# Kernel optimization log

Hardware: AMD Instinct MI355X
Metric: run time of the kernel (lower is better)

## Reference

```python
import jax, jax.numpy as jnp
import numpy as np

NUM_HEADS = 8

def _mha(x, Wq, Wk, Wv, Wo):
    # x: (..., S, C); standard multi-head self-attention, no bias, no dropout (eval mode)
    C = x.shape[-1]
    dh = C // NUM_HEADS
    lead = x.shape[:-1]
    q = (x @ Wq.T).reshape(*lead, NUM_HEADS, dh)
    k = (x @ Wk.T).reshape(*lead, NUM_HEADS, dh)
    v = (x @ Wv.T).reshape(*lead, NUM_HEADS, dh)
    scores = jnp.einsum('...qhd,...khd->...hqk', q, k) * (dh ** -0.5)
    attn = jax.nn.softmax(scores, axis=-1)
    o = jnp.einsum('...hqk,...khd->...qhd', attn, v).reshape(*lead, C)
    return o @ Wo.T

def _axial_block(xs, Wq_h, Wk_h, Wv_h, Wo_h, Wq_w, Wk_w, Wv_w, Wo_w):
    # xs: (B, C, H, W)
    # height attention: sequence along H, batched over (B, W)
    xh = jnp.transpose(xs, (0, 3, 2, 1))            # (B, W, H, C)
    oh = _mha(xh, Wq_h, Wk_h, Wv_h, Wo_h)           # (B, W, H, C)
    oh = jnp.transpose(oh, (0, 3, 2, 1))            # (B, C, H, W)
    # width attention: sequence along W, batched over (B, H)
    xw = jnp.transpose(xs, (0, 2, 3, 1))            # (B, H, W, C)
    ow = _mha(xw, Wq_w, Wk_w, Wv_w, Wo_w)           # (B, H, W, C)
    ow = jnp.transpose(ow, (0, 3, 1, 2))            # (B, C, H, W)
    return xs + oh + ow

def setup_inputs() -> dict:
    key = jax.random.key(0)
    ks = jax.random.split(key, 9)
    B, C, H, W = 8, 512, 128, 128
    s = C ** -0.5
    xs = jax.random.normal(ks[0], (B, C, H, W), dtype=jnp.float32)
    names = ['Wq_h', 'Wk_h', 'Wv_h', 'Wo_h', 'Wq_w', 'Wk_w', 'Wv_w', 'Wo_w']
    ws = {n: jax.random.normal(k, (C, C), dtype=jnp.float32) * s for n, k in zip(names, ks[1:])}
    return {'xs': xs, **ws}

def reference(xs, Wq_h, Wk_h, Wv_h, Wo_h, Wq_w, Wk_w, Wv_w, Wo_w):
    return _axial_block(xs, Wq_h, Wk_h, Wv_h, Wo_h, Wq_w, Wk_w, Wv_w, Wo_w)
```

## Files before the change

kernel.cpp:

```cpp
#include <hip/hip_runtime.h>

#define CC   512
#define HWT  16384
#define NB   8
#define DH   64
#define SEQ  128

typedef __bf16 bf16_t;
typedef __bf16 bf16x8 __attribute__((ext_vector_type(8)));
typedef float  f32x4  __attribute__((ext_vector_type(4)));

__global__ __launch_bounds__(256) void prep_w_kernel(const float* __restrict__ W0,
                                                     const float* __restrict__ W1,
                                                     const float* __restrict__ W2,
                                                     const float* __restrict__ W3,
                                                     const float* __restrict__ W4,
                                                     const float* __restrict__ W5,
                                                     const float* __restrict__ W6,
                                                     const float* __restrict__ W7,
                                                     bf16_t* __restrict__ Wb) {
  const float* Wsrc[8] = {W0, W1, W2, W3, W4, W5, W6, W7};
  const int w = blockIdx.y;
  const int i = (blockIdx.x * 256 + threadIdx.x) * 4;
  float4 v = *(const float4*)(Wsrc[w] + i);
  bf16_t* o = Wb + (size_t)w * (CC * CC) + i;
  o[0] = (bf16_t)v.x; o[1] = (bf16_t)v.y; o[2] = (bf16_t)v.z; o[3] = (bf16_t)v.w;
}

__global__ __launch_bounds__(256) void t0_kernel(const float* __restrict__ xs,
                                                 bf16_t* __restrict__ Xt) {
  __shared__ bf16_t T[64 * 72];
  const int hw0 = blockIdx.x * 64, c0 = blockIdx.y * 64;
  const size_t boff = (size_t)blockIdx.z * CC * HWT;
  const int t = threadIdx.x;
  for (int p = 0; p < 4; p++) {
    int job = t + p * 256;
    int c_l = job >> 4, ch = job & 15;
    float4 v = *(const float4*)(xs + boff + (size_t)(c0 + c_l) * HWT + hw0 + ch * 4);
    T[(ch * 4 + 0) * 72 + c_l] = (bf16_t)v.x;
    T[(ch * 4 + 1) * 72 + c_l] = (bf16_t)v.y;
    T[(ch * 4 + 2) * 72 + c_l] = (bf16_t)v.z;
    T[(ch * 4 + 3) * 72 + c_l] = (bf16_t)v.w;
  }
  __syncthreads();
  for (int p = 0; p < 2; p++) {
    int job = t + p * 256;
    int hw_l = job >> 3, ch = job & 7;
    uint4 v = *(const uint4*)&T[hw_l * 72 + ch * 8];
    *(uint4*)(Xt + boff + (size_t)(hw0 + hw_l) * CC + c0 + ch * 8) = v;
  }
}

__global__ __launch_bounds__(256) void gemm_kernel(const bf16_t* __restrict__ A,
                                                   const bf16_t* __restrict__ Wt,
                                                   bf16_t* __restrict__ D) {
  __shared__ bf16_t As[128 * 40];
  __shared__ bf16_t Ws[128 * 40];
  const int m0 = blockIdx.x * 128, n0 = blockIdx.y * 128;
  const size_t boff = (size_t)blockIdx.z * HWT * CC;
  const bf16_t* Ab = A + boff;
  bf16_t* Db = D + boff;
  const int t = threadIdx.x;
  const int lane = t & 63, wv = t >> 6;
  const int wy = wv >> 1, wx = wv & 1;
  const int r_l = t >> 2, kcol = (t & 3) * 8;
  const int ln15 = lane & 15, q8 = (lane >> 4) * 8;

  f32x4 acc[4][4];
  for (int i = 0; i < 4; i++)
    for (int j = 0; j < 4; j++) acc[i][j] = {0.f, 0.f, 0.f, 0.f};

  for (int kb = 0; kb < 16; kb++) {
    const int kk = kb * 32 + kcol;
    uint4 a0 = *(const uint4*)(Ab + (size_t)(m0 + r_l) * CC + kk);
    uint4 a1 = *(const uint4*)(Ab + (size_t)(m0 + r_l + 64) * CC + kk);
    uint4 w0 = *(const uint4*)(Wt + (size_t)(n0 + r_l) * CC + kk);
    uint4 w1 = *(const uint4*)(Wt + (size_t)(n0 + r_l + 64) * CC + kk);
    __syncthreads();
    *(uint4*)&As[r_l * 40 + kcol] = a0;
    *(uint4*)&As[(r_l + 64) * 40 + kcol] = a1;
    *(uint4*)&Ws[r_l * 40 + kcol] = w0;
    *(uint4*)&Ws[(r_l + 64) * 40 + kcol] = w1;
    __syncthreads();
    bf16x8 af[4], wf[4];
    for (int i = 0; i < 4; i++)
      af[i] = *(const bf16x8*)&As[(wy * 64 + i * 16 + ln15) * 40 + q8];
    for (int j = 0; j < 4; j++)
      wf[j] = *(const bf16x8*)&Ws[(wx * 64 + j * 16 + ln15) * 40 + q8];
    for (int i = 0; i < 4; i++)
      for (int j = 0; j < 4; j++)
        acc[i][j] = __builtin_amdgcn_mfma_f32_16x16x32_bf16(af[i], wf[j], acc[i][j], 0, 0, 0);
  }

  const int qr = (lane >> 4) * 4;
  for (int i = 0; i < 4; i++)
    for (int j = 0; j < 4; j++) {
      const int row = m0 + wy * 64 + i * 16 + qr;
      const int col = n0 + wx * 64 + j * 16 + ln15;
      for (int r = 0; r < 4; r++)
        Db[(size_t)(row + r) * CC + col] = (bf16_t)acc[i][j][r];
    }
}

__global__ __launch_bounds__(256) void attn_kernel(const bf16_t* __restrict__ Q,
                                                   const bf16_t* __restrict__ K,
                                                   const bf16_t* __restrict__ V,
                                                   bf16_t* __restrict__ O,
                                                   int seq_stride, int o_stride) {
  __shared__ bf16_t smem[128 * 72 * 2 + 64 * 136];
  bf16_t* Qs = smem;
  bf16_t* Ks = smem + 128 * 72;
  bf16_t* Vs = smem + 2 * 128 * 72;
  bf16_t* Ps = smem;

  const int o = blockIdx.x, head = blockIdx.y;
  const size_t base = (size_t)blockIdx.z * HWT * CC + (size_t)o * o_stride + head * 64;
  const int t = threadIdx.x, lane = t & 63, wv = t >> 6;
  const int ln15 = lane & 15, q = lane >> 4;

  for (int p = 0; p < 4; p++) {
    int job = t + p * 256;
    int s = job >> 3, ch = job & 7;
    uint4 qv = *(const uint4*)(Q + base + (size_t)s * seq_stride + ch * 8);
    uint4 kv = *(const uint4*)(K + base + (size_t)s * seq_stride + ch * 8);
    *(uint4*)&Qs[s * 72 + ch * 8] = qv;
    *(uint4*)&Ks[s * 72 + ch * 8] = kv;
  }
  for (int p = 0; p < 4; p++) {
    int job = t + p * 256;
    int s = job >> 3, ch = job & 7;
    uint4 vv = *(const uint4*)(V + base + (size_t)s * seq_stride + ch * 8);
    const bf16_t* e = (const bf16_t*)&vv;
    for (int jj = 0; jj < 8; jj++) Vs[(ch * 8 + jj) * 136 + s] = e[jj];
  }
  __syncthreads();

  f32x4 sacc[2][8];
  for (int i = 0; i < 2; i++)
    for (int j = 0; j < 8; j++) sacc[i][j] = {0.f, 0.f, 0.f, 0.f};
  for (int ks = 0; ks < 2; ks++) {
    bf16x8 qf[2], kf[8];
    for (int i = 0; i < 2; i++)
      qf[i] = *(const bf16x8*)&Qs[(wv * 32 + i * 16 + ln15) * 72 + ks * 32 + q * 8];
    for (int j = 0; j < 8; j++)
      kf[j] = *(const bf16x8*)&Ks[(j * 16 + ln15) * 72 + ks * 32 + q * 8];
    for (int i = 0; i < 2; i++)
      for (int j = 0; j < 8; j++)
        sacc[i][j] = __builtin_amdgcn_mfma_f32_16x16x32_bf16(qf[i], kf[j], sacc[i][j], 0, 0, 0);
  }
  __syncthreads();

  const float scale = 0.125f;
  float linv[2][4];
  for (int i = 0; i < 2; i++)
    for (int r = 0; r < 4; r++) {
      float m = -1e30f;
      for (int j = 0; j < 8; j++) m = fmaxf(m, sacc[i][j][r]);
      for (int d = 1; d < 16; d <<= 1) m = fmaxf(m, __shfl_xor(m, d));
      m *= scale;
      float sum = 0.f;
      for (int j = 0; j < 8; j++) {
        float pv = __expf(sacc[i][j][r] * scale - m);
        sacc[i][j][r] = pv;
        sum += pv;
      }
      for (int d = 1; d < 16; d <<= 1) sum += __shfl_xor(sum, d);
      linv[i][r] = 1.f / sum;
    }
  for (int i = 0; i < 2; i++)
    for (int j = 0; j < 8; j++)
      for (int r = 0; r < 4; r++)
        Ps[(wv * 32 + i * 16 + q * 4 + r) * 136 + j * 16 + ln15] = (bf16_t)sacc[i][j][r];
  __syncthreads();

  f32x4 oacc[2][4];
  for (int i = 0; i < 2; i++)
    for (int j = 0; j < 4; j++) oacc[i][j] = {0.f, 0.f, 0.f, 0.f};
  for (int ks = 0; ks < 4; ks++) {
    bf16x8 pf[2], vf[4];
    for (int i = 0; i < 2; i++)
      pf[i] = *(const bf16x8*)&Ps[(wv * 32 + i * 16 + ln15) * 136 + ks * 32 + q * 8];
    for (int j = 0; j < 4; j++)
      vf[j] = *(const bf16x8*)&Vs[(j * 16 + ln15) * 136 + ks * 32 + q * 8];
    for (int i = 0; i < 2; i++)
      for (int j = 0; j < 4; j++)
        oacc[i][j] = __builtin_amdgcn_mfma_f32_16x16x32_bf16(pf[i], vf[j], oacc[i][j], 0, 0, 0);
  }
  for (int i = 0; i < 2; i++)
    for (int j = 0; j < 4; j++)
      for (int r = 0; r < 4; r++) {
        const int s = wv * 32 + i * 16 + q * 4 + r;
        const int d = j * 16 + ln15;
        O[base + (size_t)s * seq_stride + d] = (bf16_t)(oacc[i][j][r] * linv[i][r]);
      }
}

__global__ __launch_bounds__(256) void final_add_kernel(const float* __restrict__ xs,
                                                        const bf16_t* __restrict__ OH,
                                                        const bf16_t* __restrict__ OW,
                                                        float* __restrict__ out) {
  __shared__ float TF[64 * 65];
  const int hw0 = blockIdx.x * 64, c0 = blockIdx.y * 64;
  const size_t boff = (size_t)blockIdx.z * CC * HWT;
  const int t = threadIdx.x;
  for (int p = 0; p < 2; p++) {
    int job = t + p * 256;
    int hw_l = job >> 3, ch = job & 7;
    size_t off = boff + (size_t)(hw0 + hw_l) * CC + c0 + ch * 8;
    bf16x8 a = *(const bf16x8*)(OH + off);
    bf16x8 b = *(const bf16x8*)(OW + off);
    for (int jj = 0; jj < 8; jj++)
      TF[(ch * 8 + jj) * 65 + hw_l] = (float)a[jj] + (float)b[jj];
  }
  __syncthreads();
  for (int p = 0; p < 4; p++) {
    int job = t + p * 256;
    int c_l = job >> 4, ch = job & 15;
    size_t off = boff + (size_t)(c0 + c_l) * HWT + hw0 + ch * 4;
    float4 xv = *(const float4*)(xs + off);
    float4 ov;
    ov.x = xv.x + TF[c_l * 65 + ch * 4 + 0];
    ov.y = xv.y + TF[c_l * 65 + ch * 4 + 1];
    ov.z = xv.z + TF[c_l * 65 + ch * 4 + 2];
    ov.w = xv.w + TF[c_l * 65 + ch * 4 + 3];
    *(float4*)(out + off) = ov;
  }
}

extern "C" void kernel_launch(void* const* d_in, const int* in_sizes, int n_in,
                              void* d_out, int out_size, void* d_ws, size_t ws_size,
                              hipStream_t stream) {
  const float* xs = (const float*)d_in[0];
  float* out = (float*)d_out;

  bf16_t* Wb = (bf16_t*)d_ws;
  const size_t wbytes = (size_t)8 * CC * CC * sizeof(bf16_t);
  bf16_t* wsb = Wb + (size_t)8 * CC * CC;

  const size_t pb = (size_t)HWT * CC;
  size_t avail = (ws_size > wbytes) ? (ws_size - wbytes) : 0;
  int chunkB = (int)(avail / (6 * pb * sizeof(bf16_t)));
  if (chunkB > NB) chunkB = NB;
  if (chunkB < 1) chunkB = 1;
  const size_t R = (size_t)chunkB * pb;
  bf16_t* Xt = wsb;
  bf16_t* Qb = wsb + R;
  bf16_t* Kb = wsb + 2 * R;
  bf16_t* Vb = wsb + 3 * R;
  bf16_t* Ab = wsb + 4 * R;
  bf16_t* OH = wsb + 5 * R;

  prep_w_kernel<<<dim3(CC * CC / 1024, 8), 256, 0, stream>>>(
      (const float*)d_in[1], (const float*)d_in[2], (const float*)d_in[3],
      (const float*)d_in[4], (const float*)d_in[5], (const float*)d_in[6],
      (const float*)d_in[7], (const float*)d_in[8], Wb);
  const bf16_t* Wq_h = Wb + 0 * (size_t)CC * CC;
  const bf16_t* Wk_h = Wb + 1 * (size_t)CC * CC;
  const bf16_t* Wv_h = Wb + 2 * (size_t)CC * CC;
  const bf16_t* Wo_h = Wb + 3 * (size_t)CC * CC;
  const bf16_t* Wq_w = Wb + 4 * (size_t)CC * CC;
  const bf16_t* Wk_w = Wb + 5 * (size_t)CC * CC;
  const bf16_t* Wv_w = Wb + 6 * (size_t)CC * CC;
  const bf16_t* Wo_w = Wb + 7 * (size_t)CC * CC;

  for (int b0 = 0; b0 < NB; b0 += chunkB) {
    const int cb = (NB - b0 < chunkB) ? (NB - b0) : chunkB;
    const float* xsc = xs + (size_t)b0 * pb;
    float* outc = out + (size_t)b0 * pb;
    dim3 gT(HWT / 64, CC / 64, cb);
    dim3 gG(HWT / 128, CC / 128, cb);
    dim3 gA(128, 8, cb);
    dim3 blk(256);

    t0_kernel<<<gT, blk, 0, stream>>>(xsc, Xt);
    gemm_kernel<<<gG, blk, 0, stream>>>(Xt, Wq_h, Qb);
    gemm_kernel<<<gG, blk, 0, stream>>>(Xt, Wk_h, Kb);
    gemm_kernel<<<gG, blk, 0, stream>>>(Xt, Wv_h, Vb);
    attn_kernel<<<gA, blk, 0, stream>>>(Qb, Kb, Vb, Ab, 128 * CC, CC);
    gemm_kernel<<<gG, blk, 0, stream>>>(Ab, Wo_h, OH);
    gemm_kernel<<<gG, blk, 0, stream>>>(Xt, Wq_w, Qb);
    gemm_kernel<<<gG, blk, 0, stream>>>(Xt, Wk_w, Kb);
    gemm_kernel<<<gG, blk, 0, stream>>>(Xt, Wv_w, Vb);
    attn_kernel<<<gA, blk, 0, stream>>>(Qb, Kb, Vb, Ab, CC, 128 * CC);
    gemm_kernel<<<gG, blk, 0, stream>>>(Ab, Wo_w, Xt);
    final_add_kernel<<<gT, blk, 0, stream>>>(xsc, OH, Xt, outc);
  }
}
```

Before: 1.732 ms.

## Fuse QKV projections into one GEMM and stage tiles via global_load_lds

Merges the three separate Q, K and V projection GEMMs into one GEMM with N=1536, relying on the three bf16 weight matrices sitting next to each other in the workspace. Q, K and V are written interleaved with row stride 1536, and the attention kernel takes separate input and output strides. The GEMM now copies A and W tiles straight from global memory into LDS with global_load_lds, dropping the register round trip and the padded LDS layout. The unpadded 32-element rows risk LDS bank conflicts on the fragment reads, and a second barrier per k-step is added.

```diff
diff --git a/kernel.cpp b/kernel.cpp
--- a/kernel.cpp
+++ b/kernel.cpp
@@ -5,10 +5,16 @@
 #define NB   8
 #define DH   64
 #define SEQ  128
+#define C3   1536
 
 typedef __bf16 bf16_t;
 typedef __bf16 bf16x8 __attribute__((ext_vector_type(8)));
 typedef float  f32x4  __attribute__((ext_vector_type(4)));
+
+#define GLOAD_LDS16(g, l)                                                      \
+  __builtin_amdgcn_global_load_lds(                                            \
+      (const __attribute__((address_space(1))) void*)(g),                      \
+      (__attribute__((address_space(3))) void*)(l), 16, 0, 0)
 
 __global__ __launch_bounds__(256) void prep_w_kernel(const float* __restrict__ W0,
                                                      const float* __restrict__ W1,
@@ -53,43 +59,45 @@
 
 __global__ __launch_bounds__(256) void gemm_kernel(const bf16_t* __restrict__ A,
                                                    const bf16_t* __restrict__ Wt,
-                                                   bf16_t* __restrict__ D) {
-  __shared__ bf16_t As[128 * 40];
-  __shared__ bf16_t Ws[128 * 40];
+                                                   bf16_t* __restrict__ D,
+                                                   int ldD) {
+  __shared__ bf16_t As[128 * 32];
+  __shared__ bf16_t Ws[128 * 32];
   const int m0 = blockIdx.x * 128, n0 = blockIdx.y * 128;
-  const size_t boff = (size_t)blockIdx.z * HWT * CC;
-  const bf16_t* Ab = A + boff;
-  bf16_t* Db = D + boff;
+  const bf16_t* Ab = A + (size_t)blockIdx.z * HWT * CC;
+  bf16_t* Db = D + (size_t)blockIdx.z * HWT * (size_t)ldD;
   const int t = threadIdx.x;
   const int lane = t & 63, wv = t >> 6;
   const int wy = wv >> 1, wx = wv & 1;
-  const int r_l = t >> 2, kcol = (t & 3) * 8;
   const int ln15 = lane & 15, q8 = (lane >> 4) * 8;
+
+  const int seg0 = wv * 2;
+  const int srow = lane >> 2;
+  const int scol = (lane & 3) * 8;
 
   f32x4 acc[4][4];
   for (int i = 0; i < 4; i++)
     for (int j = 0; j < 4; j++) acc[i][j] = {0.f, 0.f, 0.f, 0.f};
 
   for (int kb = 0; kb < 16; kb++) {
-    const int kk = kb * 32 + kcol;
-    uint4 a0 = *(const uint4*)(Ab + (size_t)(m0 + r_l) * CC + kk);
-    uint4 a1 = *(const uint4*)(Ab + (size_t)(m0 + r_l + 64) * CC + kk);
-    uint4 w0 = *(const uint4*)(Wt + (size_t)(n0 + r_l) * CC + kk);
-    uint4 w1 = *(const uint4*)(Wt + (size_t)(n0 + r_l + 64) * CC + kk);
-    __syncthreads();
-    *(uint4*)&As[r_l * 40 + kcol] = a0;
-    *(uint4*)&As[(r_l + 64) * 40 + kcol] = a1;
-    *(uint4*)&Ws[r_l * 40 + kcol] = w0;
-    *(uint4*)&Ws[(r_l + 64) * 40 + kcol] = w1;
+    const int kk = kb * 32;
+#pragma unroll
+    for (int i = 0; i < 2; i++) {
+      const int seg = seg0 + i;
+      const int row = seg * 16 + srow;
+      GLOAD_LDS16(Ab + (size_t)(m0 + row) * CC + kk + scol, &As[seg * 512]);
+      GLOAD_LDS16(Wt + (size_t)(n0 + row) * CC + kk + scol, &Ws[seg * 512]);
+    }
     __syncthreads();
     bf16x8 af[4], wf[4];
     for (int i = 0; i < 4; i++)
-      af[i] = *(const bf16x8*)&As[(wy * 64 + i * 16 + ln15) * 40 + q8];
+      af[i] = *(const bf16x8*)&As[(wy * 64 + i * 16 + ln15) * 32 + q8];
     for (int j = 0; j < 4; j++)
-      wf[j] = *(const bf16x8*)&Ws[(wx * 64 + j * 16 + ln15) * 40 + q8];
+      wf[j] = *(const bf16x8*)&Ws[(wx * 64 + j * 16 + ln15) * 32 + q8];
     for (int i = 0; i < 4; i++)
       for (int j = 0; j < 4; j++)
         acc[i][j] = __builtin_amdgcn_mfma_f32_16x16x32_bf16(af[i], wf[j], acc[i][j], 0, 0, 0);
+    __syncthreads();
   }
 
   const int qr = (lane >> 4) * 4;
@@ -98,7 +106,7 @@
       const int row = m0 + wy * 64 + i * 16 + qr;
       const int col = n0 + wx * 64 + j * 16 + ln15;
       for (int r = 0; r < 4; r++)
-        Db[(size_t)(row + r) * CC + col] = (bf16_t)acc[i][j][r];
+        Db[(size_t)(row + r) * ldD + col] = (bf16_t)acc[i][j][r];
     }
 }
 
@@ -106,7 +114,8 @@
                                                    const bf16_t* __restrict__ K,
                                                    const bf16_t* __restrict__ V,
                                                    bf16_t* __restrict__ O,
-                                                   int seq_stride, int o_stride) {
+                                                   int in_ss, int in_os, int in_bs,
+                                                   int out_ss, int out_os, int out_bs) {
   __shared__ bf16_t smem[128 * 72 * 2 + 64 * 136];
   bf16_t* Qs = smem;
   bf16_t* Ks = smem + 128 * 72;
@@ -114,22 +123,23 @@
   bf16_t* Ps = smem;
 
   const int o = blockIdx.x, head = blockIdx.y;
-  const size_t base = (size_t)blockIdx.z * HWT * CC + (size_t)o * o_stride + head * 64;
+  const size_t ibase = (size_t)blockIdx.z * in_bs + (size_t)o * in_os + head * 64;
+  const size_t obase = (size_t)blockIdx.z * out_bs + (size_t)o * out_os + head * 64;
   const int t = threadIdx.x, lane = t & 63, wv = t >> 6;
   const int ln15 = lane & 15, q = lane >> 4;
 
   for (int p = 0; p < 4; p++) {
     int job = t + p * 256;
     int s = job >> 3, ch = job & 7;
-    uint4 qv = *(const uint4*)(Q + base + (size_t)s * seq_stride + ch * 8);
-    uint4 kv = *(const uint4*)(K + base + (size_t)s * seq_stride + ch * 8);
+    uint4 qv = *(const uint4*)(Q + ibase + (size_t)s * in_ss + ch * 8);
+    uint4 kv = *(const uint4*)(K + ibase + (size_t)s * in_ss + ch * 8);
     *(uint4*)&Qs[s * 72 + ch * 8] = qv;
     *(uint4*)&Ks[s * 72 + ch * 8] = kv;
   }
   for (int p = 0; p < 4; p++) {
     int job = t + p * 256;
     int s = job >> 3, ch = job & 7;
-    uint4 vv = *(const uint4*)(V + base + (size_t)s * seq_stride + ch * 8);
+    uint4 vv = *(const uint4*)(V + ibase + (size_t)s * in_ss + ch * 8);
     const bf16_t* e = (const bf16_t*)&vv;
     for (int jj = 0; jj < 8; jj++) Vs[(ch * 8 + jj) * 136 + s] = e[jj];
   }
@@ -191,7 +201,7 @@
       for (int r = 0; r < 4; r++) {
         const int s = wv * 32 + i * 16 + q * 4 + r;
         const int d = j * 16 + ln15;
-        O[base + (size_t)s * seq_stride + d] = (bf16_t)(oacc[i][j][r] * linv[i][r]);
+        O[obase + (size_t)s * out_ss + d] = (bf16_t)(oacc[i][j][r] * linv[i][r]);
       }
 }
 
@@ -243,46 +253,41 @@
   if (chunkB > NB) chunkB = NB;
   if (chunkB < 1) chunkB = 1;
   const size_t R = (size_t)chunkB * pb;
-  bf16_t* Xt = wsb;
-  bf16_t* Qb = wsb + R;
-  bf16_t* Kb = wsb + 2 * R;
-  bf16_t* Vb = wsb + 3 * R;
-  bf16_t* Ab = wsb + 4 * R;
-  bf16_t* OH = wsb + 5 * R;
+  bf16_t* Xt  = wsb;
+  bf16_t* QKV = wsb + R;
+  bf16_t* Ab  = wsb + 4 * R;
+  bf16_t* OH  = wsb + 5 * R;
 
   prep_w_kernel<<<dim3(CC * CC / 1024, 8), 256, 0, stream>>>(
       (const float*)d_in[1], (const float*)d_in[2], (const float*)d_in[3],
       (const float*)d_in[4], (const float*)d_in[5], (const float*)d_in[6],
       (const float*)d_in[7], (const float*)d_in[8], Wb);
-  const bf16_t* Wq_h = Wb + 0 * (size_t)CC * CC;
-  const bf16_t* Wk_h = Wb + 1 * (size_t)CC * CC;
-  const bf16_t* Wv_h = Wb + 2 * (size_t)CC * CC;
-  const bf16_t* Wo_h = Wb + 3 * (size_t)CC * CC;
-  const bf16_t* Wq_w = Wb + 4 * (size_t)CC * CC;
-  const bf16_t* Wk_w = Wb + 5 * (size_t)CC * CC;
-  const bf16_t* Wv_w = Wb + 6 * (size_t)CC * CC;
-  const bf16_t* Wo_w = Wb + 7 * (size_t)CC * CC;
+  const bf16_t* Wqkv_h = Wb + 0 * (size_t)CC * CC;
+  const bf16_t* Wo_h   = Wb + 3 * (size_t)CC * CC;
+  const bf16_t* Wqkv_w = Wb + 4 * (size_t)CC * CC;
+  const bf16_t* Wo_w   = Wb + 7 * (size_t)CC * CC;
 
   for (int b0 = 0; b0 < NB; b0 += chunkB) {
     const int cb = (NB - b0 < chunkB) ? (NB - b0) : chunkB;
     const float* xsc = xs + (size_t)b0 * pb;
     float* outc = out + (size_t)b0 * pb;
     dim3 gT(HWT / 64, CC / 64, cb);
-    dim3 gG(HWT / 128, CC / 128, cb);
+    dim3 gQKV(HWT / 128, C3 / 128, cb);
+    dim3 gO(HWT / 128, CC / 128, cb);
     dim3 gA(128, 8, cb);
     dim3 blk(256);
 
     t0_kernel<<<gT, blk, 0, stream>>>(xsc, Xt);
-    gemm_kernel<<<gG, blk, 0, stream>>>(Xt, Wq_h, Qb);
-    gemm_kernel<<<gG, blk, 0, stream>>>(Xt, Wk_h, Kb);
-    gemm_kernel<<<gG, blk, 0, stream>>>(Xt, Wv_h, Vb);
-    attn_kernel<<<gA, blk, 0, stream>>>(Qb, Kb, Vb, Ab, 128 * CC, CC);
-    gemm_kernel<<<gG, blk, 0, stream>>>(Ab, Wo_h, OH);
-    gemm_kernel<<<gG, blk, 0, stream>>>(Xt, Wq_w, Qb);
-    gemm_kernel<<<gG, blk, 0, stream>>>(Xt, Wk_w, Kb);
-    gemm_kernel<<<gG, blk, 0, stream>>>(Xt, Wv_w, Vb);
-    attn_kernel<<<gA, blk, 0, stream>>>(Qb, Kb, Vb, Ab, CC, 128 * CC);
-    gemm_kernel<<<gG, blk, 0, stream>>>(Ab, Wo_w, Xt);
+    gemm_kernel<<<gQKV, blk, 0, stream>>>(Xt, Wqkv_h, QKV, C3);
+    attn_kernel<<<gA, blk, 0, stream>>>(QKV, QKV + 512, QKV + 1024, Ab,
+                                        128 * C3, C3, HWT * C3,
+                                        128 * CC, CC, HWT * CC);
+    gemm_kernel<<<gO, blk, 0, stream>>>(Ab, Wo_h, OH, CC);
+    gemm_kernel<<<gQKV, blk, 0, stream>>>(Xt, Wqkv_w, QKV, C3);
+    attn_kernel<<<gA, blk, 0, stream>>>(QKV, QKV + 512, QKV + 1024, Ab,
+                                        C3, 128 * C3, HWT * C3,
+                                        CC, 128 * CC, HWT * CC);
+    gemm_kernel<<<gO, blk, 0, stream>>>(Ab, Wo_w, Xt, CC);
     final_add_kernel<<<gT, blk, 0, stream>>>(xsc, OH, Xt, outc);
   }
 }
```

Result: faster. 1.629 ms (-5.9%).
